# Optimization experiments

Hardware: AMD Instinct MI355X
Metric: run time of the kernel (lower is better)

Reference implementation:

```python
import jax, jax.numpy as jnp
import numpy as np

INPUT_SIZE = 512
HIDDEN_SIZE = 512
BATCH = 16384


def setup_inputs() -> dict:
    key = jax.random.key(0)
    ks = jax.random.split(key, 11)
    stdv = 1.0 / np.sqrt(HIDDEN_SIZE)
    in_dim = INPUT_SIZE + HIDDEN_SIZE

    def unif(k, shape):
        return jax.random.uniform(k, shape, jnp.float32, -stdv, stdv)

    inp = {
        "input_": jax.random.normal(ks[0], (BATCH, INPUT_SIZE), jnp.float32),
        "prev_h": jax.random.normal(ks[1], (BATCH, HIDDEN_SIZE), jnp.float32),
        "prev_c": jax.random.normal(ks[2], (BATCH, HIDDEN_SIZE), jnp.float32),
        # gate weights in torch nn.Linear layout: (out=hidden, in=input+hidden)
        "W_i": unif(ks[3], (HIDDEN_SIZE, in_dim)),
        "b_i": unif(ks[4], (HIDDEN_SIZE,)),
        "W_f": unif(ks[5], (HIDDEN_SIZE, in_dim)),
        "b_f": unif(ks[6], (HIDDEN_SIZE,)),
        "W_g": unif(ks[7], (HIDDEN_SIZE, in_dim)),
        "b_g": unif(ks[8], (HIDDEN_SIZE,)),
        "W_o": unif(ks[9], (HIDDEN_SIZE, in_dim)),
        "b_o": unif(ks[10], (HIDDEN_SIZE,)),
    }
    return inp


def reference(input_, prev_h, prev_c, W_i, b_i, W_f, b_f, W_g, b_g, W_o, b_o):
    # x_stack = cat((prev_h, input_), dim=1)  -> (batch, hidden+input)
    x_stack = jnp.concatenate([prev_h, input_], axis=1)
    # Fuse the four gate GEMMs into one: stack weights along out dim.
    W = jnp.concatenate([W_i, W_f, W_o, W_g], axis=0)          # (4H, H+I)
    b = jnp.concatenate([b_i, b_f, b_o, b_g], axis=0)          # (4H,)
    gates = x_stack @ W.T + b                                   # (batch, 4H)
    H = prev_h.shape[1]
    i = jax.nn.sigmoid(gates[:, 0 * H:1 * H])
    f = jax.nn.sigmoid(gates[:, 1 * H:2 * H])
    o = jax.nn.sigmoid(gates[:, 2 * H:3 * H])
    g = jnp.tanh(gates[:, 3 * H:4 * H])
    c = f * prev_c + i * g
    h = jnp.tanh(c) * o
    return (h, c)
```

## Files before the change

kernel.cpp:

```cpp
#include <hip/hip_runtime.h>
#include <hip/hip_bf16.h>
#include <math.h>

typedef unsigned short u16;

#define BATCH 16384
#define HID   512
#define KDIM  1024
#define BM    128
#define BNG   128
#define NSTEP 16

typedef __bf16 bf16x8 __attribute__((ext_vector_type(8)));
typedef float  floatx4 __attribute__((ext_vector_type(4)));

__device__ __forceinline__ void async_copy16(const void* g, void* l) {
  __builtin_amdgcn_global_load_lds(
      (const __attribute__((address_space(1))) void*)g,
      (__attribute__((address_space(3))) void*)l, 16, 0, 0);
}

__device__ __forceinline__ float fast_sigmoid(float x) {
  return 1.0f / (1.0f + __expf(-x));
}
__device__ __forceinline__ float fast_tanh(float x) {
  float e = __expf(-2.0f * fabsf(x));
  float t = (1.0f - e) / (1.0f + e);
  return x >= 0.0f ? t : -t;
}
__device__ __forceinline__ u16 f2bf(float f) {
  return __builtin_bit_cast(u16, __float2bfloat16(f));
}

__global__ __launch_bounds__(256) void pack_kernel(
    const float* __restrict__ input_, const float* __restrict__ prev_h,
    const float* __restrict__ Wi, const float* __restrict__ Wf_,
    const float* __restrict__ Wo, const float* __restrict__ Wg,
    u16* __restrict__ Xb, u16* __restrict__ Wf) {
  int blk = blockIdx.x;
  int k = threadIdx.x * 4;
  if (blk < BATCH) {
    const float* src = (k < HID) ? (prev_h + (size_t)blk * HID + k)
                                 : (input_ + (size_t)blk * HID + (k - HID));
    float4 v = *(const float4*)src;
    ushort4 o;
    o.x = f2bf(v.x); o.y = f2bf(v.y); o.z = f2bf(v.z); o.w = f2bf(v.w);
    *(ushort4*)(Xb + (size_t)blk * KDIM + k) = o;
  } else {
    int grow = blk - BATCH;
    int g = grow >> 9;
    int n = grow & (HID - 1);
    const float* s = g == 0 ? Wi : g == 1 ? Wf_ : g == 2 ? Wo : Wg;
    float4 v = *(const float4*)(s + (size_t)n * KDIM + k);
    ushort4 o;
    o.x = f2bf(v.x); o.y = f2bf(v.y); o.z = f2bf(v.z); o.w = f2bf(v.w);
    size_t d = ((size_t)((g * 32 + (n >> 4)) * 32 + (k >> 5)) * 64 +
                ((k >> 3) & 3) * 16 + (n & 15)) * 8 + (k & 7);
    *(ushort4*)(Wf + d) = o;
  }
}

__global__ __launch_bounds__(512, 2) void lstm_gemm_kernel(
    const u16* __restrict__ Xb, const u16* __restrict__ Wf,
    const float* __restrict__ Bi, const float* __restrict__ Bf,
    const float* __restrict__ Bo, const float* __restrict__ Bg,
    const float* __restrict__ prevC, float* __restrict__ out) {
  __shared__ u16 lds[2][8192];

  const int tid = threadIdx.x;
  const int wave = tid >> 6, lane = tid & 63;
  const int lrow = lane & 15, lquad = lane >> 4;
  const int m_block = blockIdx.x * BM;
  const int ntg = blockIdx.y * 8 + wave;

  const int swz = ((lane & 7) ^ ((lane >> 3) & 7)) * 8;
  const u16* gp[2];
  int lp[2];
#pragma unroll
  for (int i = 0; i < 2; ++i) {
    int li = wave * 2 + i;
    gp[i] = Xb + (size_t)(m_block + li * 8 + (lane >> 3)) * KDIM + swz;
    lp[i] = li * 512;
  }

  floatx4 acc[4][8];
#pragma unroll
  for (int g = 0; g < 4; ++g)
#pragma unroll
    for (int mt = 0; mt < 8; ++mt)
      acc[g][mt] = (floatx4){0.f, 0.f, 0.f, 0.f};

  auto fill = [&](int buf, int S) {
#pragma unroll
    for (int i = 0; i < 2; ++i)
      async_copy16(gp[i] + S * 64, &lds[0][0] + buf * 8192 + lp[i]);
  };

  auto loadB = [&](int S, bf16x8 (&dst)[2][4]) {
#pragma unroll
    for (int kk = 0; kk < 2; ++kk)
#pragma unroll
      for (int g = 0; g < 4; ++g)
        dst[kk][g] = *(const bf16x8*)(
            Wf + (((size_t)(g * 32 + ntg) * 32 + (S * 2 + kk)) << 9) +
            lane * 8);
  };

  auto compute = [&](int buf, bf16x8 (&B)[2][4]) {
    const u16* LA = &lds[buf][0];
#pragma unroll
    for (int kk = 0; kk < 2; ++kk) {
#pragma unroll
      for (int mt = 0; mt < 8; ++mt) {
        bf16x8 a = *(const bf16x8*)
            &LA[(mt * 16 + lrow) * 64 + (((kk * 4 + lquad) ^ (lrow & 7)) * 8)];
#pragma unroll
        for (int g = 0; g < 4; ++g)
          acc[g][mt] = __builtin_amdgcn_mfma_f32_16x16x32_bf16(
              a, B[kk][g], acc[g][mt], 0, 0, 0);
      }
    }
  };

  bf16x8 b0[2][4], b1[2][4];
  loadB(0, b0);
  fill(0, 0);
  for (int S = 0; S < NSTEP; S += 2) {
    __syncthreads();
    fill(1, S + 1);
    loadB(S + 1 < NSTEP ? S + 1 : S, b1);
    compute(0, b0);
    __syncthreads();
    if (S + 2 < NSTEP) {
      fill(0, S + 2);
      loadB(S + 2, b0);
    }
    compute(1, b1);
  }

  const int j = ntg * 16 + lrow;
  const float vbi = Bi[j], vbf = Bf[j], vbo = Bo[j], vbg = Bg[j];
  float* outH = out;
  float* outC = out + (size_t)BATCH * HID;
#pragma unroll
  for (int mt = 0; mt < 8; ++mt) {
    int rowb = m_block + mt * 16 + lquad * 4;
#pragma unroll
    for (int r = 0; r < 4; ++r) {
      int row = rowb + r;
      float gi = fast_sigmoid(acc[0][mt][r] + vbi);
      float gf = fast_sigmoid(acc[1][mt][r] + vbf);
      float go = fast_sigmoid(acc[2][mt][r] + vbo);
      float gg = fast_tanh(acc[3][mt][r] + vbg);
      float c = gf * prevC[row * HID + j] + gi * gg;
      float h = fast_tanh(c) * go;
      outH[row * HID + j] = h;
      outC[row * HID + j] = c;
    }
  }
}

__global__ void lstm_fallback_kernel(
    const float* __restrict__ input_, const float* __restrict__ prev_h,
    const float* __restrict__ prevC,
    const float* __restrict__ Wi, const float* __restrict__ Bi,
    const float* __restrict__ Wf, const float* __restrict__ Bf,
    const float* __restrict__ Wo, const float* __restrict__ Bo,
    const float* __restrict__ Wg, const float* __restrict__ Bg,
    float* __restrict__ out) {
  int idx = blockIdx.x * blockDim.x + threadIdx.x;
  int b = idx / HID, j = idx % HID;
  if (b >= BATCH) return;
  float si = 0.f, sf = 0.f, so = 0.f, sg = 0.f;
  for (int k = 0; k < KDIM; ++k) {
    float x = (k < HID) ? prev_h[b * HID + k] : input_[b * HID + (k - HID)];
    si += x * Wi[j * KDIM + k];
    sf += x * Wf[j * KDIM + k];
    so += x * Wo[j * KDIM + k];
    sg += x * Wg[j * KDIM + k];
  }
  float gi = fast_sigmoid(si + Bi[j]);
  float gf = fast_sigmoid(sf + Bf[j]);
  float go = fast_sigmoid(so + Bo[j]);
  float gg = fast_tanh(sg + Bg[j]);
  float c = gf * prevC[b * HID + j] + gi * gg;
  out[b * HID + j] = fast_tanh(c) * go;
  out[(size_t)BATCH * HID + b * HID + j] = c;
}

extern "C" void kernel_launch(void* const* d_in, const int* in_sizes, int n_in,
                              void* d_out, int out_size, void* d_ws, size_t ws_size,
                              hipStream_t stream) {
  const float* input_ = (const float*)d_in[0];
  const float* prev_h = (const float*)d_in[1];
  const float* prev_c = (const float*)d_in[2];
  const float* W_i = (const float*)d_in[3];
  const float* b_i = (const float*)d_in[4];
  const float* W_f = (const float*)d_in[5];
  const float* b_f = (const float*)d_in[6];
  const float* W_g = (const float*)d_in[7];
  const float* b_g = (const float*)d_in[8];
  const float* W_o = (const float*)d_in[9];
  const float* b_o = (const float*)d_in[10];
  float* out = (float*)d_out;

  const size_t ws_needed =
      (size_t)BATCH * KDIM * sizeof(u16) + (size_t)4 * HID * KDIM * sizeof(u16);

  if (ws_size < ws_needed) {
    int total = BATCH * HID;
    lstm_fallback_kernel<<<(total + 255) / 256, 256, 0, stream>>>(
        input_, prev_h, prev_c, W_i, b_i, W_f, b_f, W_o, b_o, W_g, b_g, out);
    return;
  }

  u16* Xb = (u16*)d_ws;
  u16* Wf = Xb + (size_t)BATCH * KDIM;

  pack_kernel<<<BATCH + 4 * HID, 256, 0, stream>>>(input_, prev_h,
                                                   W_i, W_f, W_o, W_g, Xb, Wf);

  dim3 grid(BATCH / BM, HID / BNG);
  lstm_gemm_kernel<<<grid, 512, 0, stream>>>(Xb, Wf, b_i, b_f, b_o, b_g,
                                             prev_c, out);
}
```

Baseline: 242.9 us.

## Fuse activation fp32-to-bf16 conversion into GEMM A-tile loads

```diff
diff --git a/kernel.cpp b/kernel.cpp
--- a/kernel.cpp
+++ b/kernel.cpp
@@ -8,17 +8,10 @@
 #define HID   512
 #define KDIM  1024
 #define BM    128
-#define BNG   128
 #define NSTEP 16
 
 typedef __bf16 bf16x8 __attribute__((ext_vector_type(8)));
 typedef float  floatx4 __attribute__((ext_vector_type(4)));
-
-__device__ __forceinline__ void async_copy16(const void* g, void* l) {
-  __builtin_amdgcn_global_load_lds(
-      (const __attribute__((address_space(1))) void*)g,
-      (__attribute__((address_space(3))) void*)l, 16, 0, 0);
-}
 
 __device__ __forceinline__ float fast_sigmoid(float x) {
   return 1.0f / (1.0f + __expf(-x));
@@ -32,36 +25,26 @@
   return __builtin_bit_cast(u16, __float2bfloat16(f));
 }
 
-__global__ __launch_bounds__(256) void pack_kernel(
-    const float* __restrict__ input_, const float* __restrict__ prev_h,
+__global__ __launch_bounds__(256) void pack_w_kernel(
     const float* __restrict__ Wi, const float* __restrict__ Wf_,
     const float* __restrict__ Wo, const float* __restrict__ Wg,
-    u16* __restrict__ Xb, u16* __restrict__ Wf) {
-  int blk = blockIdx.x;
+    u16* __restrict__ Wf) {
+  int grow = blockIdx.x;
   int k = threadIdx.x * 4;
-  if (blk < BATCH) {
-    const float* src = (k < HID) ? (prev_h + (size_t)blk * HID + k)
-                                 : (input_ + (size_t)blk * HID + (k - HID));
-    float4 v = *(const float4*)src;
-    ushort4 o;
-    o.x = f2bf(v.x); o.y = f2bf(v.y); o.z = f2bf(v.z); o.w = f2bf(v.w);
-    *(ushort4*)(Xb + (size_t)blk * KDIM + k) = o;
-  } else {
-    int grow = blk - BATCH;
-    int g = grow >> 9;
-    int n = grow & (HID - 1);
-    const float* s = g == 0 ? Wi : g == 1 ? Wf_ : g == 2 ? Wo : Wg;
-    float4 v = *(const float4*)(s + (size_t)n * KDIM + k);
-    ushort4 o;
-    o.x = f2bf(v.x); o.y = f2bf(v.y); o.z = f2bf(v.z); o.w = f2bf(v.w);
-    size_t d = ((size_t)((g * 32 + (n >> 4)) * 32 + (k >> 5)) * 64 +
-                ((k >> 3) & 3) * 16 + (n & 15)) * 8 + (k & 7);
-    *(ushort4*)(Wf + d) = o;
-  }
+  int g = grow >> 9;
+  int n = grow & (HID - 1);
+  const float* s = g == 0 ? Wi : g == 1 ? Wf_ : g == 2 ? Wo : Wg;
+  float4 v = *(const float4*)(s + (size_t)n * KDIM + k);
+  ushort4 o;
+  o.x = f2bf(v.x); o.y = f2bf(v.y); o.z = f2bf(v.z); o.w = f2bf(v.w);
+  size_t d = ((size_t)((g * 32 + (n >> 4)) * 32 + (k >> 5)) * 64 +
+              ((k >> 3) & 3) * 16 + (n & 15)) * 8 + (k & 7);
+  *(ushort4*)(Wf + d) = o;
 }
 
 __global__ __launch_bounds__(512, 2) void lstm_gemm_kernel(
-    const u16* __restrict__ Xb, const u16* __restrict__ Wf,
+    const float* __restrict__ input_, const float* __restrict__ prev_h,
+    const u16* __restrict__ Wf,
     const float* __restrict__ Bi, const float* __restrict__ Bf,
     const float* __restrict__ Bo, const float* __restrict__ Bg,
     const float* __restrict__ prevC, float* __restrict__ out) {
@@ -73,14 +56,17 @@
   const int m_block = blockIdx.x * BM;
   const int ntg = blockIdx.y * 8 + wave;
 
-  const int swz = ((lane & 7) ^ ((lane >> 3) & 7)) * 8;
-  const u16* gp[2];
+  const int swzf = ((lane & 7) ^ ((lane >> 3) & 7)) * 8;
+  const float* xh[2];
+  const float* xi[2];
   int lp[2];
 #pragma unroll
   for (int i = 0; i < 2; ++i) {
     int li = wave * 2 + i;
-    gp[i] = Xb + (size_t)(m_block + li * 8 + (lane >> 3)) * KDIM + swz;
-    lp[i] = li * 512;
+    int row = m_block + li * 8 + (lane >> 3);
+    xh[i] = prev_h + (size_t)row * HID + swzf;
+    xi[i] = input_ + (size_t)row * HID + swzf;
+    lp[i] = li * 512 + lane * 8;
   }
 
   floatx4 acc[4][8];
@@ -90,23 +76,40 @@
     for (int mt = 0; mt < 8; ++mt)
       acc[g][mt] = (floatx4){0.f, 0.f, 0.f, 0.f};
 
-  auto fill = [&](int buf, int S) {
-#pragma unroll
-    for (int i = 0; i < 2; ++i)
-      async_copy16(gp[i] + S * 64, &lds[0][0] + buf * 8192 + lp[i]);
-  };
-
-  auto loadB = [&](int S, bf16x8 (&dst)[2][4]) {
+  float4 r[2][2];
+  auto ldX = [&](int S) {
+#pragma unroll
+    for (int i = 0; i < 2; ++i) {
+      const float* base = (S < 8) ? (xh[i] + S * 64) : (xi[i] + (S - 8) * 64);
+      r[i][0] = *(const float4*)(base);
+      r[i][1] = *(const float4*)(base + 4);
+    }
+  };
+
+  auto cvtWrite = [&](int buf) {
+#pragma unroll
+    for (int i = 0; i < 2; ++i) {
+      union { u16 u[8]; bf16x8 v; } t;
+      t.u[0] = f2bf(r[i][0].x); t.u[1] = f2bf(r[i][0].y);
+      t.u[2] = f2bf(r[i][0].z); t.u[3] = f2bf(r[i][0].w);
+      t.u[4] = f2bf(r[i][1].x); t.u[5] = f2bf(r[i][1].y);
+      t.u[6] = f2bf(r[i][1].z); t.u[7] = f2bf(r[i][1].w);
+      *(bf16x8*)(&lds[buf][lp[i]]) = t.v;
+    }
+  };
+
+  bf16x8 b[2][4];
+  auto loadB = [&](int S) {
 #pragma unroll
     for (int kk = 0; kk < 2; ++kk)
 #pragma unroll
       for (int g = 0; g < 4; ++g)
-        dst[kk][g] = *(const bf16x8*)(
+        b[kk][g] = *(const bf16x8*)(
             Wf + (((size_t)(g * 32 + ntg) * 32 + (S * 2 + kk)) << 9) +
             lane * 8);
   };
 
-  auto compute = [&](int buf, bf16x8 (&B)[2][4]) {
+  auto compute = [&](int buf) {
     const u16* LA = &lds[buf][0];
 #pragma unroll
     for (int kk = 0; kk < 2; ++kk) {
@@ -117,25 +120,25 @@
 #pragma unroll
         for (int g = 0; g < 4; ++g)
           acc[g][mt] = __builtin_amdgcn_mfma_f32_16x16x32_bf16(
-              a, B[kk][g], acc[g][mt], 0, 0, 0);
+              a, b[kk][g], acc[g][mt], 0, 0, 0);
       }
     }
   };
 
-  bf16x8 b0[2][4], b1[2][4];
-  loadB(0, b0);
-  fill(0, 0);
-  for (int S = 0; S < NSTEP; S += 2) {
+  loadB(0);
+  ldX(0);
+  cvtWrite(0);
+  __syncthreads();
+
+  for (int S = 0; S < NSTEP; ++S) {
+    const int buf = S & 1;
+    if (S + 1 < NSTEP) ldX(S + 1);
+    compute(buf);
+    if (S + 1 < NSTEP) {
+      loadB(S + 1);
+      cvtWrite(buf ^ 1);
+    }
     __syncthreads();
-    fill(1, S + 1);
-    loadB(S + 1 < NSTEP ? S + 1 : S, b1);
-    compute(0, b0);
-    __syncthreads();
-    if (S + 2 < NSTEP) {
-      fill(0, S + 2);
-      loadB(S + 2, b0);
-    }
-    compute(1, b1);
   }
 
   const int j = ntg * 16 + lrow;
@@ -146,12 +149,12 @@
   for (int mt = 0; mt < 8; ++mt) {
     int rowb = m_block + mt * 16 + lquad * 4;
 #pragma unroll
-    for (int r = 0; r < 4; ++r) {
-      int row = rowb + r;
-      float gi = fast_sigmoid(acc[0][mt][r] + vbi);
-      float gf = fast_sigmoid(acc[1][mt][r] + vbf);
-      float go = fast_sigmoid(acc[2][mt][r] + vbo);
-      float gg = fast_tanh(acc[3][mt][r] + vbg);
+    for (int rg = 0; rg < 4; ++rg) {
+      int row = rowb + rg;
+      float gi = fast_sigmoid(acc[0][mt][rg] + vbi);
+      float gf = fast_sigmoid(acc[1][mt][rg] + vbf);
+      float go = fast_sigmoid(acc[2][mt][rg] + vbo);
+      float gg = fast_tanh(acc[3][mt][rg] + vbg);
       float c = gf * prevC[row * HID + j] + gi * gg;
       float h = fast_tanh(c) * go;
       outH[row * HID + j] = h;
@@ -204,8 +207,7 @@
   const float* b_o = (const float*)d_in[10];
   float* out = (float*)d_out;
 
-  const size_t ws_needed =
-      (size_t)BATCH * KDIM * sizeof(u16) + (size_t)4 * HID * KDIM * sizeof(u16);
+  const size_t ws_needed = (size_t)4 * HID * KDIM * sizeof(u16);
 
   if (ws_size < ws_needed) {
     int total = BATCH * HID;
@@ -214,13 +216,11 @@
     return;
   }
 
-  u16* Xb = (u16*)d_ws;
-  u16* Wf = Xb + (size_t)BATCH * KDIM;
-
-  pack_kernel<<<BATCH + 4 * HID, 256, 0, stream>>>(input_, prev_h,
-                                                   W_i, W_f, W_o, W_g, Xb, Wf);
-
-  dim3 grid(BATCH / BM, HID / BNG);
-  lstm_gemm_kernel<<<grid, 512, 0, stream>>>(Xb, Wf, b_i, b_f, b_o, b_g,
-                                             prev_c, out);
-}
+  u16* Wfp = (u16*)d_ws;
+
+  pack_w_kernel<<<4 * HID, 256, 0, stream>>>(W_i, W_f, W_o, W_g, Wfp);
+
+  dim3 grid(BATCH / BM, HID / 128);
+  lstm_gemm_kernel<<<grid, 512, 0, stream>>>(input_, prev_h, Wfp,
+                                             b_i, b_f, b_o, b_g, prev_c, out);
+}
```

Result: faster. 223.4 us (-8.0%).

## Retile GEMM to 2x4 wave grid, single-buffer B, raise occupancy

Applied to the files above, without the earlier changes.

```diff
diff --git a/kernel.cpp b/kernel.cpp
--- a/kernel.cpp
+++ b/kernel.cpp
@@ -8,7 +8,6 @@
 #define HID   512
 #define KDIM  1024
 #define BM    128
-#define BNG   128
 #define NSTEP 16
 
 typedef __bf16 bf16x8 __attribute__((ext_vector_type(8)));
@@ -60,7 +59,7 @@
   }
 }
 
-__global__ __launch_bounds__(512, 2) void lstm_gemm_kernel(
+__global__ __launch_bounds__(512, 4) void lstm_gemm_kernel(
     const u16* __restrict__ Xb, const u16* __restrict__ Wf,
     const float* __restrict__ Bi, const float* __restrict__ Bf,
     const float* __restrict__ Bo, const float* __restrict__ Bg,
@@ -70,8 +69,9 @@
   const int tid = threadIdx.x;
   const int wave = tid >> 6, lane = tid & 63;
   const int lrow = lane & 15, lquad = lane >> 4;
-  const int m_block = blockIdx.x * BM;
-  const int ntg = blockIdx.y * 8 + wave;
+  const int wr = wave >> 2, wc = wave & 3;
+  const int m_block = blockIdx.y * BM;
+  const int ntg = blockIdx.x * 4 + wc;
 
   const int swz = ((lane & 7) ^ ((lane >> 3) & 7)) * 8;
   const u16* gp[2];
@@ -83,11 +83,11 @@
     lp[i] = li * 512;
   }
 
-  floatx4 acc[4][8];
+  floatx4 acc[4][4];
 #pragma unroll
   for (int g = 0; g < 4; ++g)
 #pragma unroll
-    for (int mt = 0; mt < 8; ++mt)
+    for (int mt = 0; mt < 4; ++mt)
       acc[g][mt] = (floatx4){0.f, 0.f, 0.f, 0.f};
 
   auto fill = [&](int buf, int S) {
@@ -96,46 +96,47 @@
       async_copy16(gp[i] + S * 64, &lds[0][0] + buf * 8192 + lp[i]);
   };
 
-  auto loadB = [&](int S, bf16x8 (&dst)[2][4]) {
+  bf16x8 b[2][4];
+  auto loadB = [&](int S) {
 #pragma unroll
     for (int kk = 0; kk < 2; ++kk)
 #pragma unroll
       for (int g = 0; g < 4; ++g)
-        dst[kk][g] = *(const bf16x8*)(
+        b[kk][g] = *(const bf16x8*)(
             Wf + (((size_t)(g * 32 + ntg) * 32 + (S * 2 + kk)) << 9) +
             lane * 8);
   };
 
-  auto compute = [&](int buf, bf16x8 (&B)[2][4]) {
+  auto compute = [&](int buf) {
     const u16* LA = &lds[buf][0];
+    __builtin_amdgcn_s_setprio(1);
 #pragma unroll
     for (int kk = 0; kk < 2; ++kk) {
 #pragma unroll
-      for (int mt = 0; mt < 8; ++mt) {
+      for (int mt = 0; mt < 4; ++mt) {
         bf16x8 a = *(const bf16x8*)
-            &LA[(mt * 16 + lrow) * 64 + (((kk * 4 + lquad) ^ (lrow & 7)) * 8)];
+            &LA[(wr * 64 + mt * 16 + lrow) * 64 +
+                (((kk * 4 + lquad) ^ (lrow & 7)) * 8)];
 #pragma unroll
         for (int g = 0; g < 4; ++g)
           acc[g][mt] = __builtin_amdgcn_mfma_f32_16x16x32_bf16(
-              a, B[kk][g], acc[g][mt], 0, 0, 0);
+              a, b[kk][g], acc[g][mt], 0, 0, 0);
       }
     }
+    __builtin_amdgcn_s_setprio(0);
   };
 
-  bf16x8 b0[2][4], b1[2][4];
-  loadB(0, b0);
   fill(0, 0);
-  for (int S = 0; S < NSTEP; S += 2) {
-    __syncthreads();
-    fill(1, S + 1);
-    loadB(S + 1 < NSTEP ? S + 1 : S, b1);
-    compute(0, b0);
-    __syncthreads();
-    if (S + 2 < NSTEP) {
-      fill(0, S + 2);
-      loadB(S + 2, b0);
-    }
-    compute(1, b1);
+  loadB(0);
+
+  for (int S = 0; S < NSTEP; ++S) {
+    const int buf = S & 1;
+    asm volatile("s_waitcnt vmcnt(8) lgkmcnt(0)" ::: "memory");
+    __builtin_amdgcn_s_barrier();
+    __builtin_amdgcn_sched_barrier(0);
+    if (S + 1 < NSTEP) fill(buf ^ 1, S + 1);
+    compute(buf);
+    if (S + 1 < NSTEP) loadB(S + 1);
   }
 
   const int j = ntg * 16 + lrow;
@@ -143,15 +144,15 @@
   float* outH = out;
   float* outC = out + (size_t)BATCH * HID;
 #pragma unroll
-  for (int mt = 0; mt < 8; ++mt) {
-    int rowb = m_block + mt * 16 + lquad * 4;
-#pragma unroll
-    for (int r = 0; r < 4; ++r) {
-      int row = rowb + r;
-      float gi = fast_sigmoid(acc[0][mt][r] + vbi);
-      float gf = fast_sigmoid(acc[1][mt][r] + vbf);
-      float go = fast_sigmoid(acc[2][mt][r] + vbo);
-      float gg = fast_tanh(acc[3][mt][r] + vbg);
+  for (int mt = 0; mt < 4; ++mt) {
+    int rowb = m_block + wr * 64 + mt * 16 + lquad * 4;
+#pragma unroll
+    for (int rg = 0; rg < 4; ++rg) {
+      int row = rowb + rg;
+      float gi = fast_sigmoid(acc[0][mt][rg] + vbi);
+      float gf = fast_sigmoid(acc[1][mt][rg] + vbf);
+      float go = fast_sigmoid(acc[2][mt][rg] + vbo);
+      float gg = fast_tanh(acc[3][mt][rg] + vbg);
       float c = gf * prevC[row * HID + j] + gi * gg;
       float h = fast_tanh(c) * go;
       outH[row * HID + j] = h;
@@ -215,12 +216,12 @@
   }
 
   u16* Xb = (u16*)d_ws;
-  u16* Wf = Xb + (size_t)BATCH * KDIM;
+  u16* Wfp = Xb + (size_t)BATCH * KDIM;
 
   pack_kernel<<<BATCH + 4 * HID, 256, 0, stream>>>(input_, prev_h,
-                                                   W_i, W_f, W_o, W_g, Xb, Wf);
-
-  dim3 grid(BATCH / BM, HID / BNG);
-  lstm_gemm_kernel<<<grid, 512, 0, stream>>>(Xb, Wf, b_i, b_f, b_o, b_g,
+                                                   W_i, W_f, W_o, W_g, Xb, Wfp);
+
+  dim3 grid(8, BATCH / BM);
+  lstm_gemm_kernel<<<grid, 512, 0, stream>>>(Xb, Wfp, b_i, b_f, b_o, b_g,
                                              prev_c, out);
 }
```

New measurement: 241.7 us. Within noise of the previous version (-0.5%).
